# Performance work log

Measured on AMD Instinct MI355X. Metric: run time of the kernel, lower is better.

Reference implementation:

```python
import jax, jax.numpy as jnp
import numpy as np

B, T, C = 4, 2048, 768   # batch, seq, n_embd
E, K = 8, 2              # n_routed_experts, moe_top_k (expert hidden dim == C per source)


def setup_inputs() -> dict:
    key = jax.random.key(0)
    ks = jax.random.split(key, 6)
    s = 0.02  # init scale to keep relu(x)^2 well-behaved
    return {
        "x": jax.random.normal(ks[0], (B, T, C), jnp.float32),
        "w_fc_sh": jax.random.normal(ks[1], (C, C), jnp.float32) * s,    # shared expert c_fc (stored [in,out])
        "w_proj_sh": jax.random.normal(ks[2], (C, C), jnp.float32) * s,  # shared expert c_proj
        "w1": jax.random.normal(ks[3], (E, C, C), jnp.float32) * s,      # routed experts c_fc, [E,in,out]
        "w2": jax.random.normal(ks[4], (E, C, C), jnp.float32) * s,      # routed experts c_proj
        "router_w": jax.random.normal(ks[5], (E, C), jnp.float32) * s,   # router weight [E, C]
        "balance_bias": jnp.zeros((E,), jnp.float32),                    # router balance_bias buffer
    }


def _mlp(x, wfc, wproj):
    # MLP: c_proj(relu(c_fc(x))**2)
    h = jnp.square(jax.nn.relu(x @ wfc))
    return h @ wproj


def reference(x, w_fc_sh, w_proj_sh, w1, w2, router_w, balance_bias):
    Bx, Tx, Cx = x.shape
    shared = _mlp(x, w_fc_sh, w_proj_sh)                    # [B,T,C]

    xf = x.reshape(-1, Cx)                                  # [N,C]
    # --- router ---
    logits = xf.astype(jnp.float32) @ router_w.T            # [N,E]
    scores = jax.nn.sigmoid(logits)
    _, idx = jax.lax.top_k(scores + balance_bias, K)        # selection uses biased scores
    tw = jnp.take_along_axis(scores, idx, axis=-1)          # gate weights from unbiased scores
    tw = tw / (tw.sum(-1, keepdims=True) + 1e-20)           # [N,K]

    # per-token per-expert combine weights (equivalent to gather/MLP/index_add loop)
    combine = (jax.nn.one_hot(idx, E, dtype=tw.dtype) * tw[..., None]).sum(1)  # [N,E]

    # dense all-expert compute, masked combine (same math as sparse dispatch)
    h = jnp.square(jax.nn.relu(jnp.einsum('nc,ech->neh', xf, w1)))  # [N,E,H]
    y = jnp.einsum('neh,ehc->nec', h, w2)                            # [N,E,C]
    routed = jnp.einsum('nec,ne->nc', y, combine)                    # [N,C]

    return shared + routed.reshape(Bx, Tx, Cx)
```

## Files before the change

kernel.cpp:

```cpp
#include <hip/hip_runtime.h>
#include <stdint.h>

#define N_TOK 8192
#define C_DIM 768
#define E_NUM 8
#define NT2 (C_DIM / 64)
#define TOTX 200
#define GRID1 1200
#define XXPX 25

typedef short short8 __attribute__((ext_vector_type(8)));
typedef __bf16 bf16x8 __attribute__((ext_vector_type(8)));
typedef float f32x4 __attribute__((ext_vector_type(4)));

static __device__ __forceinline__ unsigned short f2bf(float f) {
    unsigned u = __float_as_uint(f);
    unsigned r = u + 0x7FFFu + ((u >> 16) & 1u);
    return (unsigned short)(r >> 16);
}
static __device__ __forceinline__ float bf2f(unsigned short h) {
    return __uint_as_float(((unsigned)h) << 16);
}

__global__ void wtrans_kernel(const float* __restrict__ wfc, const float* __restrict__ wpj,
                              const float* __restrict__ w1, const float* __restrict__ w2,
                              unsigned short* __restrict__ Wt) {
    __shared__ float tile[32][33];
    const int m = blockIdx.z;
    const float* src = (m == 0) ? wfc : (m == 1) ? wpj
                     : (m < 10) ? (w1 + (size_t)(m - 2) * C_DIM * C_DIM)
                                : (w2 + (size_t)(m - 10) * C_DIM * C_DIM);
    const int i0 = blockIdx.y * 32;
    const int o0 = blockIdx.x * 32;
    #pragma unroll
    for (int rr = 0; rr < 32; rr += 8)
        tile[threadIdx.y + rr][threadIdx.x] = src[(size_t)(i0 + threadIdx.y + rr) * C_DIM + o0 + threadIdx.x];
    __syncthreads();
    unsigned short* dst = Wt + (size_t)m * C_DIM * C_DIM;
    #pragma unroll
    for (int rr = 0; rr < 32; rr += 8) {
        int o = o0 + threadIdx.y + rr;
        dst[(size_t)o * C_DIM + i0 + threadIdx.x] = f2bf(tile[threadIdx.x][threadIdx.y + rr]);
    }
}

__global__ void router_kernel(const float* __restrict__ x, const float* __restrict__ rw,
                              const float* __restrict__ bias,
                              float* __restrict__ topk_w, int* __restrict__ eids,
                              unsigned short* __restrict__ xb) {
    const int wave = threadIdx.x >> 6;
    const int lane = threadIdx.x & 63;
    const int n = blockIdx.x * 4 + wave;
    const float* xp = x + (size_t)n * C_DIM + lane * 12;
    float xv[12];
    #pragma unroll
    for (int j = 0; j < 12; j++) xv[j] = xp[j];
    unsigned short* xbp = xb + (size_t)n * C_DIM + lane * 12;
    #pragma unroll
    for (int j = 0; j < 12; j++) xbp[j] = f2bf(xv[j]);
    float acc[E_NUM];
    #pragma unroll
    for (int e = 0; e < E_NUM; e++) acc[e] = 0.f;
    #pragma unroll
    for (int e = 0; e < E_NUM; e++) {
        const float* wp = rw + (size_t)e * C_DIM + lane * 12;
        #pragma unroll
        for (int j = 0; j < 12; j++) acc[e] += xv[j] * wp[j];
    }
    #pragma unroll
    for (int e = 0; e < E_NUM; e++) {
        #pragma unroll
        for (int off = 32; off > 0; off >>= 1) acc[e] += __shfl_xor(acc[e], off, 64);
    }
    if (lane == 0) {
        float sc[E_NUM];
        #pragma unroll
        for (int e = 0; e < E_NUM; e++) sc[e] = 1.f / (1.f + expf(-acc[e]));
        int e0 = 0; float best = -1e30f;
        #pragma unroll
        for (int e = 0; e < E_NUM; e++) { float v = sc[e] + bias[e]; if (v > best) { best = v; e0 = e; } }
        int e1 = -1; float best1 = -1e30f;
        #pragma unroll
        for (int e = 0; e < E_NUM; e++) { if (e == e0) continue; float v = sc[e] + bias[e]; if (v > best1) { best1 = v; e1 = e; } }
        float w0 = sc[e0], w1 = sc[e1];
        float s = w0 + w1 + 1e-20f;
        w0 /= s; w1 /= s;
        topk_w[n * 2] = w0; topk_w[n * 2 + 1] = w1;
        eids[n * 2] = e0; eids[n * 2 + 1] = e1;
    }
}

__global__ __launch_bounds__(1024) void bucketize_kernel(const int* __restrict__ eids,
                                                         int* __restrict__ counts,
                                                         int* __restrict__ buckets) {
    const int e = blockIdx.x;
    const int t = threadIdx.x;
    const int wv = t >> 6, lane = t & 63;
    __shared__ int wave_tot[16];
    int running = 0;
    for (int start = 0; start < 2 * N_TOK; start += 1024) {
        const int i = start + t;
        const int f = (eids[i] == e) ? 1 : 0;
        unsigned long long mask = __ballot(f);
        int pre = __popcll(mask & ((1ull << lane) - 1ull));
        if (lane == 0) wave_tot[wv] = __popcll(mask);
        __syncthreads();
        int wbase = 0, tot = 0;
        #pragma unroll
        for (int j = 0; j < 16; j++) { int c = wave_tot[j]; tot += c; if (j < wv) wbase += c; }
        if (f) buckets[e * N_TOK + running + wbase + pre] = i;
        running += tot;
        __syncthreads();
    }
    if (t == 0) counts[e] = running;
}

__global__ void prefix_kernel(const int* __restrict__ counts, int* __restrict__ xoffs) {
    if (threadIdx.x == 0 && blockIdx.x == 0) {
        int a = 0;
        for (int z = 0; z < E_NUM; z++) { xoffs[z] = a; a += (counts[z] + 127) >> 7; }
        xoffs[E_NUM] = a;
        xoffs[E_NUM + 1] = a + 64;
    }
}

#define GLOAD_LDS(g, l) __builtin_amdgcn_global_load_lds((const __attribute__((address_space(1))) void*)(g), (__attribute__((address_space(3))) void*)(l), 16, 0, 0)
#define WAITVM0() asm volatile("s_waitcnt vmcnt(0)" ::: "memory")
#define SCHEDB() __builtin_amdgcn_sched_barrier(0)
#define BAR() __builtin_amdgcn_s_barrier()

template <int PHASE>
__global__ __launch_bounds__(256, 2) void gemm_all_kernel(const unsigned short* __restrict__ Adir,
                                                          const unsigned short* __restrict__ Agat,
                                                          const unsigned short* __restrict__ WtAll,
                                                          void* __restrict__ dstDir,
                                                          unsigned short* __restrict__ dstGat,
                                                          const int* __restrict__ counts,
                                                          const int* __restrict__ buckets,
                                                          const int* __restrict__ xoffs) {
    const int fid = blockIdx.x;
    const int xcd = fid & 7;
    const int i6 = fid >> 3;
    const int xx = xcd * XXPX + i6 / 6;
    const int y = i6 % 6;
    int xo[10];
    #pragma unroll
    for (int i = 0; i < 10; i++) xo[i] = xoffs[i];
    if (xx >= xo[9]) return;
    int z = E_NUM, xl = xx - xo[8];
    #pragma unroll
    for (int zz = 0; zz < E_NUM; zz++)
        if (xx >= xo[zz] && xx < xo[zz + 1]) { z = zz; xl = xx - xo[zz]; }
    const bool sh = (z == E_NUM);
    const int rows = sh ? N_TOK : counts[z];
    const int r0 = xl * 128;
    const int c0 = y * 128;

    __shared__ __align__(16) unsigned short lds[2 * 16384];

    const int t = threadIdx.x;
    const int lane = t & 63;
    const int wv = t >> 6;
    const int wr = (wv >> 1) * 64;
    const int wc = (wv & 1) * 64;

    const int widx = sh ? (PHASE == 0 ? 0 : 1) : (PHASE == 0 ? 2 + z : 10 + z);
    const unsigned short* Bmat = WtAll + (size_t)widx * C_DIM * C_DIM;
    const int* bk = buckets + z * N_TOK;

    const int srow = t >> 3;
    const int scol = (((t & 7) ^ ((t >> 3) & 7)) * 8);
    int grow[4];
    const unsigned short* Asrc;
    if (sh) {
        Asrc = Adir;
        #pragma unroll
        for (int c = 0; c < 4; c++) grow[c] = r0 + 32 * c + srow;
    } else {
        Asrc = Agat;
        #pragma unroll
        for (int c = 0; c < 4; c++) {
            int p = r0 + 32 * c + srow;
            int ev = bk[p < rows ? p : 0];
            grow[c] = (PHASE == 0) ? (ev >> 1) : ev;
        }
    }
    const unsigned short* ap[4];
    const unsigned short* bp[4];
    #pragma unroll
    for (int c = 0; c < 4; c++) {
        ap[c] = Asrc + (size_t)grow[c] * C_DIM + scol;
        bp[c] = Bmat + (size_t)(c0 + 32 * c + srow) * C_DIM + scol;
    }

    f32x4 acc[4][4];
    #pragma unroll
    for (int i = 0; i < 4; i++)
        #pragma unroll
        for (int j = 0; j < 4; j++) acc[i][j] = (f32x4){0.f, 0.f, 0.f, 0.f};

    const int fr = lane & 15;
    const int fq = lane >> 4;
    const int ks0 = ((fq ^ (fr & 7)) * 8);
    const int ks1 = (((4 + fq) ^ (fr & 7)) * 8);

    {
        unsigned short* d = lds + t * 8;
        #pragma unroll
        for (int c = 0; c < 4; c++) {
            GLOAD_LDS(ap[c], d + c * 2048);
            GLOAD_LDS(bp[c], d + 8192 + c * 2048);
        }
    }

    #pragma unroll
    for (int kt = 0; kt < NT2; ++kt) {
        WAITVM0();
        BAR();
        SCHEDB();
        if (kt + 1 < NT2) {
            unsigned short* d = lds + ((kt + 1) & 1) * 16384 + t * 8;
            const int ko = (kt + 1) * 64;
            #pragma unroll
            for (int c = 0; c < 4; c++) {
                GLOAD_LDS(ap[c] + ko, d + c * 2048);
                GLOAD_LDS(bp[c] + ko, d + 8192 + c * 2048);
            }
        }
        SCHEDB();
        const unsigned short* buf = lds + (kt & 1) * 16384;
        short8 af[4][2], bfr[4][2];
        #pragma unroll
        for (int i = 0; i < 4; i++) {
            const unsigned short* rp = buf + (size_t)(wr + i * 16 + fr) * 64;
            af[i][0] = *reinterpret_cast<const short8*>(rp + ks0);
            af[i][1] = *reinterpret_cast<const short8*>(rp + ks1);
        }
        #pragma unroll
        for (int j = 0; j < 4; j++) {
            const unsigned short* rp = buf + 8192 + (size_t)(wc + j * 16 + fr) * 64;
            bfr[j][0] = *reinterpret_cast<const short8*>(rp + ks0);
            bfr[j][1] = *reinterpret_cast<const short8*>(rp + ks1);
        }
        __builtin_amdgcn_s_setprio(1);
        #pragma unroll
        for (int kk = 0; kk < 2; kk++)
            #pragma unroll
            for (int i = 0; i < 4; i++)
                #pragma unroll
                for (int j = 0; j < 4; j++)
                    acc[i][j] = __builtin_amdgcn_mfma_f32_16x16x32_bf16(
                        __builtin_bit_cast(bf16x8, af[i][kk]), __builtin_bit_cast(bf16x8, bfr[j][kk]),
                        acc[i][j], 0, 0, 0);
        __builtin_amdgcn_s_setprio(0);
    }

    if (sh) {
        if constexpr (PHASE == 0) {
            unsigned short* Hd = (unsigned short*)dstDir;
            #pragma unroll
            for (int i = 0; i < 4; i++)
                #pragma unroll
                for (int rr = 0; rr < 4; rr++) {
                    int n = r0 + wr + i * 16 + fq * 4 + rr;
                    size_t base = (size_t)n * C_DIM;
                    #pragma unroll
                    for (int j = 0; j < 4; j++) {
                        int col = c0 + wc + j * 16 + fr;
                        float v = acc[i][j][rr];
                        float rl = v > 0.f ? v : 0.f;
                        Hd[base + col] = f2bf(rl * rl);
                    }
                }
        } else {
            float* od = (float*)dstDir;
            #pragma unroll
            for (int i = 0; i < 4; i++)
                #pragma unroll
                for (int rr = 0; rr < 4; rr++) {
                    int n = r0 + wr + i * 16 + fq * 4 + rr;
                    size_t base = (size_t)n * C_DIM;
                    #pragma unroll
                    for (int j = 0; j < 4; j++) {
                        int col = c0 + wc + j * 16 + fr;
                        od[base + col] = acc[i][j][rr];
                    }
                }
        }
    } else {
        #pragma unroll
        for (int i = 0; i < 4; i++)
            #pragma unroll
            for (int rr = 0; rr < 4; rr++) {
                int pos = r0 + wr + i * 16 + fq * 4 + rr;
                if (pos < rows) {
                    int ent = bk[pos];
                    size_t base = (size_t)ent * C_DIM;
                    #pragma unroll
                    for (int j = 0; j < 4; j++) {
                        int col = c0 + wc + j * 16 + fr;
                        float v = acc[i][j][rr];
                        if (PHASE == 0) {
                            float rl = v > 0.f ? v : 0.f;
                            dstGat[base + col] = f2bf(rl * rl);
                        } else {
                            dstGat[base + col] = f2bf(v);
                        }
                    }
                }
            }
    }
}

__global__ void combine_kernel(float* __restrict__ out, const unsigned short* __restrict__ Y,
                               const float* __restrict__ tw) {
    int idx = blockIdx.x * blockDim.x + threadIdx.x;
    const int per_row = C_DIM / 4;
    if (idx >= N_TOK * per_row) return;
    int n = idx / per_row;
    int c = (idx % per_row) * 4;
    float w0 = tw[n * 2], w1 = tw[n * 2 + 1];
    const ushort4 a = *reinterpret_cast<const ushort4*>(Y + (size_t)(n * 2) * C_DIM + c);
    const ushort4 b = *reinterpret_cast<const ushort4*>(Y + (size_t)(n * 2 + 1) * C_DIM + c);
    float4* op = reinterpret_cast<float4*>(out + (size_t)n * C_DIM + c);
    float4 o = *op;
    o.x += w0 * bf2f(a.x) + w1 * bf2f(b.x);
    o.y += w0 * bf2f(a.y) + w1 * bf2f(b.y);
    o.z += w0 * bf2f(a.z) + w1 * bf2f(b.z);
    o.w += w0 * bf2f(a.w) + w1 * bf2f(b.w);
    *op = o;
}

extern "C" void kernel_launch(void* const* d_in, const int* in_sizes, int n_in,
                              void* d_out, int out_size, void* d_ws, size_t ws_size,
                              hipStream_t stream) {
    const float* x   = (const float*)d_in[0];
    const float* wfc = (const float*)d_in[1];
    const float* wpj = (const float*)d_in[2];
    const float* w1  = (const float*)d_in[3];
    const float* w2  = (const float*)d_in[4];
    const float* rw  = (const float*)d_in[5];
    const float* bias= (const float*)d_in[6];
    float* out = (float*)d_out;

    char* ws = (char*)d_ws;
    size_t off = 0;
    auto alloc = [&](size_t bytes) { void* p = ws + off; off += (bytes + 255) & ~(size_t)255; return p; };
    unsigned short* xb   = (unsigned short*)alloc((size_t)N_TOK * C_DIM * 2);
    unsigned short* Wt   = (unsigned short*)alloc((size_t)18 * C_DIM * C_DIM * 2);
    unsigned short* H    = (unsigned short*)alloc((size_t)N_TOK * 2 * C_DIM * 2);
    unsigned short* Hsh  = (unsigned short*)alloc((size_t)N_TOK * C_DIM * 2);
    unsigned short* Y    = (unsigned short*)alloc((size_t)N_TOK * 2 * C_DIM * 2);
    float* topk_w        = (float*)alloc((size_t)N_TOK * 2 * 4);
    int* counts          = (int*)alloc(256);
    int* buckets         = (int*)alloc((size_t)E_NUM * N_TOK * 4);
    int* eids            = (int*)alloc((size_t)2 * N_TOK * 4);
    int* xoffs           = (int*)alloc(64);

    wtrans_kernel<<<dim3(24, 24, 18), dim3(32, 8), 0, stream>>>(wfc, wpj, w1, w2, Wt);
    router_kernel<<<N_TOK / 4, 256, 0, stream>>>(x, rw, bias, topk_w, eids, xb);
    bucketize_kernel<<<E_NUM, 1024, 0, stream>>>(eids, counts, buckets);
    prefix_kernel<<<1, 64, 0, stream>>>(counts, xoffs);

    gemm_all_kernel<0><<<GRID1, 256, 0, stream>>>(xb, xb, Wt, Hsh, H, counts, buckets, xoffs);
    gemm_all_kernel<1><<<GRID1, 256, 0, stream>>>(Hsh, H, Wt, out, Y, counts, buckets, xoffs);

    combine_kernel<<<(N_TOK * (C_DIM / 4) + 255) / 256, 256, 0, stream>>>(out, Y, topk_w);
}
```

Baseline: 140.2 us.

## Enlarge expert GEMM tiles to 256x256 with eight-wave workgroups

Both grouped GEMM phases move from 128x128 output tiles with 4 waves to 256x256 tiles with 8 waves, each wave computing a 128x64 sub-tile. Expert row blocks are rounded to 256 tokens and the grid shrinks accordingly. A-fragments are now loaded from LDS inside the MFMA loop to save registers. The goal is more operand reuse per byte loaded into LDS. The cost is a doubled LDS footprint (128KB), which likely allows only one block per CU, plus more padding rows per expert and a coarser grid of about 312 blocks that may leave CUs idle in a tail.

Result: slower. 156.8 us (+11.9%).

```diff
diff --git a/kernel.cpp b/kernel.cpp
--- a/kernel.cpp
+++ b/kernel.cpp
@@ -5,9 +5,9 @@
 #define C_DIM 768
 #define E_NUM 8
 #define NT2 (C_DIM / 64)
-#define TOTX 200
-#define GRID1 1200
-#define XXPX 25
+#define TOTX3 104
+#define GRID3 312
+#define XXP3 13
 
 typedef short short8 __attribute__((ext_vector_type(8)));
 typedef __bf16 bf16x8 __attribute__((ext_vector_type(8)));
@@ -118,9 +118,9 @@
 __global__ void prefix_kernel(const int* __restrict__ counts, int* __restrict__ xoffs) {
     if (threadIdx.x == 0 && blockIdx.x == 0) {
         int a = 0;
-        for (int z = 0; z < E_NUM; z++) { xoffs[z] = a; a += (counts[z] + 127) >> 7; }
+        for (int z = 0; z < E_NUM; z++) { xoffs[z] = a; a += (counts[z] + 255) >> 8; }
         xoffs[E_NUM] = a;
-        xoffs[E_NUM + 1] = a + 64;
+        xoffs[E_NUM + 1] = a + 32;
     }
 }
 
@@ -130,7 +130,7 @@
 #define BAR() __builtin_amdgcn_s_barrier()
 
 template <int PHASE>
-__global__ __launch_bounds__(256, 2) void gemm_all_kernel(const unsigned short* __restrict__ Adir,
+__global__ __launch_bounds__(512, 2) void gemm_all_kernel(const unsigned short* __restrict__ Adir,
                                                           const unsigned short* __restrict__ Agat,
                                                           const unsigned short* __restrict__ WtAll,
                                                           void* __restrict__ dstDir,
@@ -140,9 +140,9 @@
                                                           const int* __restrict__ xoffs) {
     const int fid = blockIdx.x;
     const int xcd = fid & 7;
-    const int i6 = fid >> 3;
-    const int xx = xcd * XXPX + i6 / 6;
-    const int y = i6 % 6;
+    const int i3 = fid >> 3;
+    const int xx = xcd * XXP3 + i3 / 3;
+    const int y = i3 % 3;
     int xo[10];
     #pragma unroll
     for (int i = 0; i < 10; i++) xo[i] = xoffs[i];
@@ -153,16 +153,16 @@
         if (xx >= xo[zz] && xx < xo[zz + 1]) { z = zz; xl = xx - xo[zz]; }
     const bool sh = (z == E_NUM);
     const int rows = sh ? N_TOK : counts[z];
-    const int r0 = xl * 128;
-    const int c0 = y * 128;
-
-    __shared__ __align__(16) unsigned short lds[2 * 16384];
+    const int r0 = xl * 256;
+    const int c0 = y * 256;
+
+    __shared__ __align__(16) unsigned short lds[2 * 32768];
 
     const int t = threadIdx.x;
     const int lane = t & 63;
     const int wv = t >> 6;
-    const int wr = (wv >> 1) * 64;
-    const int wc = (wv & 1) * 64;
+    const int wm = wv >> 2;
+    const int wn = wv & 3;
 
     const int widx = sh ? (PHASE == 0 ? 0 : 1) : (PHASE == 0 ? 2 + z : 10 + z);
     const unsigned short* Bmat = WtAll + (size_t)widx * C_DIM * C_DIM;
@@ -175,12 +175,12 @@
     if (sh) {
         Asrc = Adir;
         #pragma unroll
-        for (int c = 0; c < 4; c++) grow[c] = r0 + 32 * c + srow;
+        for (int c = 0; c < 4; c++) grow[c] = r0 + 64 * c + srow;
     } else {
         Asrc = Agat;
         #pragma unroll
         for (int c = 0; c < 4; c++) {
-            int p = r0 + 32 * c + srow;
+            int p = r0 + 64 * c + srow;
             int ev = bk[p < rows ? p : 0];
             grow[c] = (PHASE == 0) ? (ev >> 1) : ev;
         }
@@ -190,12 +190,12 @@
     #pragma unroll
     for (int c = 0; c < 4; c++) {
         ap[c] = Asrc + (size_t)grow[c] * C_DIM + scol;
-        bp[c] = Bmat + (size_t)(c0 + 32 * c + srow) * C_DIM + scol;
-    }
-
-    f32x4 acc[4][4];
-    #pragma unroll
-    for (int i = 0; i < 4; i++)
+        bp[c] = Bmat + (size_t)(c0 + 64 * c + srow) * C_DIM + scol;
+    }
+
+    f32x4 acc[8][4];
+    #pragma unroll
+    for (int i = 0; i < 8; i++)
         #pragma unroll
         for (int j = 0; j < 4; j++) acc[i][j] = (f32x4){0.f, 0.f, 0.f, 0.f};
 
@@ -208,8 +208,8 @@
         unsigned short* d = lds + t * 8;
         #pragma unroll
         for (int c = 0; c < 4; c++) {
-            GLOAD_LDS(ap[c], d + c * 2048);
-            GLOAD_LDS(bp[c], d + 8192 + c * 2048);
+            GLOAD_LDS(ap[c], d + c * 4096);
+            GLOAD_LDS(bp[c], d + 16384 + c * 4096);
         }
     }
 
@@ -219,92 +219,87 @@
         BAR();
         SCHEDB();
         if (kt + 1 < NT2) {
-            unsigned short* d = lds + ((kt + 1) & 1) * 16384 + t * 8;
+            unsigned short* d = lds + ((kt + 1) & 1) * 32768 + t * 8;
             const int ko = (kt + 1) * 64;
             #pragma unroll
             for (int c = 0; c < 4; c++) {
-                GLOAD_LDS(ap[c] + ko, d + c * 2048);
-                GLOAD_LDS(bp[c] + ko, d + 8192 + c * 2048);
+                GLOAD_LDS(ap[c] + ko, d + c * 4096);
+                GLOAD_LDS(bp[c] + ko, d + 16384 + c * 4096);
             }
         }
         SCHEDB();
-        const unsigned short* buf = lds + (kt & 1) * 16384;
-        short8 af[4][2], bfr[4][2];
-        #pragma unroll
-        for (int i = 0; i < 4; i++) {
-            const unsigned short* rp = buf + (size_t)(wr + i * 16 + fr) * 64;
-            af[i][0] = *reinterpret_cast<const short8*>(rp + ks0);
-            af[i][1] = *reinterpret_cast<const short8*>(rp + ks1);
-        }
+        const unsigned short* buf = lds + (kt & 1) * 32768;
+        short8 bfr[4][2];
         #pragma unroll
         for (int j = 0; j < 4; j++) {
-            const unsigned short* rp = buf + 8192 + (size_t)(wc + j * 16 + fr) * 64;
+            const unsigned short* rp = buf + 16384 + (size_t)(wn * 64 + j * 16 + fr) * 64;
             bfr[j][0] = *reinterpret_cast<const short8*>(rp + ks0);
             bfr[j][1] = *reinterpret_cast<const short8*>(rp + ks1);
         }
         __builtin_amdgcn_s_setprio(1);
         #pragma unroll
-        for (int kk = 0; kk < 2; kk++)
-            #pragma unroll
-            for (int i = 0; i < 4; i++)
-                #pragma unroll
-                for (int j = 0; j < 4; j++)
-                    acc[i][j] = __builtin_amdgcn_mfma_f32_16x16x32_bf16(
-                        __builtin_bit_cast(bf16x8, af[i][kk]), __builtin_bit_cast(bf16x8, bfr[j][kk]),
-                        acc[i][j], 0, 0, 0);
+        for (int i = 0; i < 8; i++) {
+            const unsigned short* rp = buf + (size_t)(wm * 128 + i * 16 + fr) * 64;
+            short8 a0 = *reinterpret_cast<const short8*>(rp + ks0);
+            short8 a1 = *reinterpret_cast<const short8*>(rp + ks1);
+            #pragma unroll
+            for (int j = 0; j < 4; j++)
+                acc[i][j] = __builtin_amdgcn_mfma_f32_16x16x32_bf16(
+                    __builtin_bit_cast(bf16x8, a0), __builtin_bit_cast(bf16x8, bfr[j][0]), acc[i][j], 0, 0, 0);
+            #pragma unroll
+            for (int j = 0; j < 4; j++)
+                acc[i][j] = __builtin_amdgcn_mfma_f32_16x16x32_bf16(
+                    __builtin_bit_cast(bf16x8, a1), __builtin_bit_cast(bf16x8, bfr[j][1]), acc[i][j], 0, 0, 0);
+        }
         __builtin_amdgcn_s_setprio(0);
     }
 
+    const int orow = r0 + wm * 128;
+    const int ocol = c0 + wn * 64;
     if (sh) {
         if constexpr (PHASE == 0) {
             unsigned short* Hd = (unsigned short*)dstDir;
             #pragma unroll
-            for (int i = 0; i < 4; i++)
+            for (int i = 0; i < 8; i++)
                 #pragma unroll
                 for (int rr = 0; rr < 4; rr++) {
-                    int n = r0 + wr + i * 16 + fq * 4 + rr;
-                    size_t base = (size_t)n * C_DIM;
+                    size_t base = (size_t)(orow + i * 16 + fq * 4 + rr) * C_DIM;
                     #pragma unroll
                     for (int j = 0; j < 4; j++) {
-                        int col = c0 + wc + j * 16 + fr;
                         float v = acc[i][j][rr];
                         float rl = v > 0.f ? v : 0.f;
-                        Hd[base + col] = f2bf(rl * rl);
+                        Hd[base + ocol + j * 16 + fr] = f2bf(rl * rl);
                     }
                 }
         } else {
             float* od = (float*)dstDir;
             #pragma unroll
-            for (int i = 0; i < 4; i++)
+            for (int i = 0; i < 8; i++)
                 #pragma unroll
                 for (int rr = 0; rr < 4; rr++) {
-                    int n = r0 + wr + i * 16 + fq * 4 + rr;
-                    size_t base = (size_t)n * C_DIM;
+                    size_t base = (size_t)(orow + i * 16 + fq * 4 + rr) * C_DIM;
                     #pragma unroll
-                    for (int j = 0; j < 4; j++) {
-                        int col = c0 + wc + j * 16 + fr;
-                        od[base + col] = acc[i][j][rr];
-                    }
+                    for (int j = 0; j < 4; j++)
+                        od[base + ocol + j * 16 + fr] = acc[i][j][rr];
                 }
         }
     } else {
         #pragma unroll
-        for (int i = 0; i < 4; i++)
+        for (int i = 0; i < 8; i++)
             #pragma unroll
             for (int rr = 0; rr < 4; rr++) {
-                int pos = r0 + wr + i * 16 + fq * 4 + rr;
+                int pos = orow + i * 16 + fq * 4 + rr;
                 if (pos < rows) {
                     int ent = bk[pos];
                     size_t base = (size_t)ent * C_DIM;
                     #pragma unroll
                     for (int j = 0; j < 4; j++) {
-                        int col = c0 + wc + j * 16 + fr;
                         float v = acc[i][j][rr];
                         if (PHASE == 0) {
                             float rl = v > 0.f ? v : 0.f;
-                            dstGat[base + col] = f2bf(rl * rl);
+                            dstGat[base + ocol + j * 16 + fr] = f2bf(rl * rl);
                         } else {
-                            dstGat[base + col] = f2bf(v);
+                            dstGat[base + ocol + j * 16 + fr] = f2bf(v);
                         }
                     }
                 }
@@ -362,8 +357,8 @@
     bucketize_kernel<<<E_NUM, 1024, 0, stream>>>(eids, counts, buckets);
     prefix_kernel<<<1, 64, 0, stream>>>(counts, xoffs);
 
-    gemm_all_kernel<0><<<GRID1, 256, 0, stream>>>(xb, xb, Wt, Hsh, H, counts, buckets, xoffs);
-    gemm_all_kernel<1><<<GRID1, 256, 0, stream>>>(Hsh, H, Wt, out, Y, counts, buckets, xoffs);
+    gemm_all_kernel<0><<<GRID3, 512, 0, stream>>>(xb, xb, Wt, Hsh, H, counts, buckets, xoffs);
+    gemm_all_kernel<1><<<GRID3, 512, 0, stream>>>(Hsh, H, Wt, out, Y, counts, buckets, xoffs);
 
     combine_kernel<<<(N_TOK * (C_DIM / 4) + 255) / 256, 256, 0, stream>>>(out, Y, topk_w);
 }
```
